# Performance work log

Measured on AMD Instinct MI355X. Metric: run time of the kernel, lower is better.

## Reference

```python
import jax, jax.numpy as jnp
import numpy as np

B, T, C = 4, 2048, 1024
H = 16
D = C // H  # head_dim = 64

def setup_inputs() -> dict:
    key = jax.random.key(0)
    k1, k2, k3 = jax.random.split(key, 3)
    x = jax.random.normal(k1, (B, T, C), dtype=jnp.float32)
    Wqkv = jax.random.normal(k2, (C, 3 * C), dtype=jnp.float32) * (C ** -0.5)
    Wproj = jax.random.normal(k3, (C, C), dtype=jnp.float32) * (C ** -0.5)
    return {"x": x, "Wqkv": Wqkv, "Wproj": Wproj}

def reference(x, Wqkv, Wproj):
    b, t, c = x.shape
    qkv = (x @ Wqkv).reshape(b, t, 3, H, D)
    qkv = jnp.transpose(qkv, (2, 0, 3, 1, 4))  # [3, B, H, T, D]
    q, k, v = qkv[0], qkv[1], qkv[2]
    att = jnp.einsum('bhqd,bhkd->bhqk', q, k) * (D ** -0.5)
    causal = jnp.tril(jnp.ones((t, t), dtype=bool))  # True where allowed
    att = jnp.where(causal, att, -jnp.inf)
    att = jax.nn.softmax(att, axis=-1)
    out = jnp.einsum('bhqk,bhkd->bhqd', att, v)  # [B, H, T, D]
    out = jnp.transpose(out, (0, 2, 1, 3)).reshape(b, t, c)
    return out @ Wproj
```

## Files before the change

kernel.cpp:

```cpp
#include <hip/hip_runtime.h>
#include <stdint.h>

typedef unsigned short u16;
typedef __bf16 bf16x8 __attribute__((ext_vector_type(8)));
typedef float f32x4 __attribute__((ext_vector_type(4)));

#define DEVI static __device__ __forceinline__

DEVI u16 f2bf(float f) {
  union { float f; unsigned u; } v; v.f = f;
  unsigned r = v.u + 0x7FFF + ((v.u >> 16) & 1);
  return (u16)(r >> 16);
}

DEVI unsigned pkbf(float a, float b) {
  union { float f; unsigned u; } x, y; x.f = a; y.f = b;
  return __builtin_amdgcn_perm(y.u + 0x8000u, x.u + 0x8000u, 0x07060302u);
}

DEVI unsigned cvtpk(float lo, float hi) {
  unsigned r;
  asm("v_cvt_pk_bf16_f32 %0, %1, %2" : "=v"(r) : "v"(lo), "v"(hi));
  return r;
}

DEVI void lds_fence() { asm volatile("s_waitcnt lgkmcnt(0)" ::: "memory"); }

DEVI void gl2lds16(const u16* g, u16* l) {
  __builtin_amdgcn_global_load_lds(
      (const __attribute__((address_space(1))) unsigned int*)(uintptr_t)g,
      (__attribute__((address_space(3))) unsigned int*)(uintptr_t)l,
      16, 0, 0);
}

__global__ __launch_bounds__(256)
void prep(const float* __restrict__ x, u16* __restrict__ xb,
          const float* __restrict__ Wqkv, u16* __restrict__ wqkvT,
          const float* __restrict__ Wproj, u16* __restrict__ wprojT) {
  __shared__ float tile[64][65];
  const int blk = blockIdx.x;
  if (blk < 8192) {
    const int i = blk * 256 + threadIdx.x;
    const float4 v = ((const float4*)x)[i];
    ushort4 o;
    o.x = f2bf(v.x); o.y = f2bf(v.y); o.z = f2bf(v.z); o.w = f2bf(v.w);
    ((ushort4*)xb)[i] = o;
    return;
  }
  const float* in; u16* out; int Cn, n0, r0;
  if (blk < 8960) {
    const int p = blk - 8192;
    in = Wqkv; out = wqkvT; Cn = 3072;
    n0 = (p % 48) * 64; r0 = (p / 48) * 64;
  } else {
    const int p = blk - 8960;
    in = Wproj; out = wprojT; Cn = 1024;
    n0 = (p % 16) * 64; r0 = (p / 16) * 64;
  }
#pragma unroll
  for (int i = 0; i < 16; ++i) {
    const int e = threadIdx.x + i * 256;
    const int r = e >> 6, c = e & 63;
    tile[r][c] = in[(size_t)(r0 + r) * Cn + n0 + c];
  }
  __syncthreads();
#pragma unroll
  for (int i = 0; i < 16; ++i) {
    const int e = threadIdx.x + i * 256;
    const int r = e >> 6, c = e & 63;
    out[(size_t)(n0 + r) * 1024 + r0 + c] = f2bf(tile[c][r]);
  }
}

template <int MODE>
__global__ __launch_bounds__(256)
void gemm128(const u16* __restrict__ A, const u16* __restrict__ Bt,
             int M, int N, int K, float* __restrict__ Cout,
             u16* __restrict__ Qg, u16* __restrict__ Kg, u16* __restrict__ Vtg) {
  __shared__ alignas(16) u16 As0[128 * 32];
  __shared__ alignas(16) u16 As1[128 * 32];
  __shared__ alignas(16) u16 Bs0[128 * 32];
  __shared__ alignas(16) u16 Bs1[128 * 32];
  const int tid = threadIdx.x;
  const int wave = tid >> 6, lane = tid & 63;
  const int quad = lane >> 4, l15 = lane & 15;
  const int m0 = blockIdx.y * 128;
  const int n0 = blockIdx.x * 128;
  const int wm = (wave >> 1) * 64;
  const int wn = (wave & 1) * 64;

  f32x4 acc[4][4] = {};

  const int q1 = wave * 64 + lane;
  const int q2 = q1 + 256;
  const int r1 = q1 >> 2, c1 = q1 & 3;
  const int r2 = q2 >> 2, c2 = q2 & 3;
  const size_t ga1 = (size_t)(m0 + r1) * K + c1 * 8;
  const size_t ga2 = (size_t)(m0 + r2) * K + c2 * 8;
  const size_t gb1 = (size_t)(n0 + r1) * K + c1 * 8;
  const size_t gb2 = (size_t)(n0 + r2) * K + c2 * 8;

  for (int k0 = 0; k0 < K; k0 += 64) {
    __syncthreads();
    gl2lds16(A + ga1 + k0, As0 + wave * 512);
    gl2lds16(A + ga2 + k0, As0 + 2048 + wave * 512);
    gl2lds16(Bt + gb1 + k0, Bs0 + wave * 512);
    gl2lds16(Bt + gb2 + k0, Bs0 + 2048 + wave * 512);
    gl2lds16(A + ga1 + k0 + 32, As1 + wave * 512);
    gl2lds16(A + ga2 + k0 + 32, As1 + 2048 + wave * 512);
    gl2lds16(Bt + gb1 + k0 + 32, Bs1 + wave * 512);
    gl2lds16(Bt + gb2 + k0 + 32, Bs1 + 2048 + wave * 512);
    __syncthreads();
#pragma unroll
    for (int kh = 0; kh < 2; ++kh) {
      const u16* Asl = kh ? As1 : As0;
      const u16* Bsl = kh ? Bs1 : Bs0;
      bf16x8 av[4], bv[4];
#pragma unroll
      for (int i = 0; i < 4; ++i)
        av[i] = *(const bf16x8*)(Asl + (wm + i * 16 + l15) * 32 + quad * 8);
#pragma unroll
      for (int j = 0; j < 4; ++j)
        bv[j] = *(const bf16x8*)(Bsl + (wn + j * 16 + l15) * 32 + quad * 8);
#pragma unroll
      for (int i = 0; i < 4; ++i)
#pragma unroll
        for (int j = 0; j < 4; ++j)
          acc[i][j] = __builtin_amdgcn_mfma_f32_16x16x32_bf16(av[i], bv[j], acc[i][j], 0, 0, 0);
    }
  }

  if constexpr (MODE == 0) {
#pragma unroll
    for (int i = 0; i < 4; ++i) {
#pragma unroll
      for (int j = 0; j < 4; ++j) {
        const int mb = m0 + wm + i * 16 + quad * 4;
        const int n = n0 + wn + j * 16 + l15;
#pragma unroll
        for (int r = 0; r < 4; ++r)
          Cout[(size_t)(mb + r) * N + n] = acc[i][j][r];
      }
    }
  } else {
    const int s0b = n0 >> 10;
    const int b = m0 >> 11;
    const int h = ((n0 + wn) >> 6) & 15;
    const int bh = b * 16 + h;
    const int tbase = (m0 & 2047) + wm;
    if (s0b == 2) {
      __syncthreads();
      u16* sl = (wave < 2 ? As0 : Bs0) + (wave & 1) * 2048;
#pragma unroll
      for (int jp = 0; jp < 2; ++jp) {
#pragma unroll
        for (int j2 = 0; j2 < 2; ++j2) {
          const int j = jp * 2 + j2;
          const int dl = j2 * 16 + l15;
          const int sw8 = dl & 7;
#pragma unroll
          for (int i = 0; i < 4; ++i) {
            const int tq = i * 2 + (quad >> 1);
            ushort4 pk;
            pk.x = f2bf(acc[i][j][0]); pk.y = f2bf(acc[i][j][1]);
            pk.z = f2bf(acc[i][j][2]); pk.w = f2bf(acc[i][j][3]);
            *(ushort4*)(sl + dl * 64 + ((tq ^ sw8) << 3) + (quad & 1) * 4) = pk;
          }
        }
        lds_fence();
#pragma unroll
        for (int p = 0; p < 4; ++p) {
          const int dl = p * 8 + (lane >> 3);
          const int tc = lane & 7;
          const int tcu = tc ^ (dl & 7);
          const uint4 v = *(const uint4*)(sl + dl * 64 + tc * 8);
          *(uint4*)(Vtg + ((size_t)(bh * 64 + jp * 32 + dl)) * 2048 + tbase + tcu * 8) = v;
        }
        lds_fence();
      }
    } else {
      u16* dst = s0b ? Kg : Qg;
      const float scale = s0b ? 1.0f : 0.18033688f;
#pragma unroll
      for (int i = 0; i < 4; ++i) {
        const int t0 = tbase + i * 16 + quad * 4;
#pragma unroll
        for (int j = 0; j < 4; ++j) {
          const int d = j * 16 + l15;
#pragma unroll
          for (int r = 0; r < 4; ++r)
            dst[((size_t)bh * 2048 + t0 + r) * 64 + d] = f2bf(acc[i][j][r] * scale);
        }
      }
    }
  }
}

__global__ __launch_bounds__(256)
void attn_fwd(const u16* __restrict__ Qg, const u16* __restrict__ Kg,
              const u16* __restrict__ Vtg, u16* __restrict__ Og) {
  __shared__ alignas(16) u16 Ks[2][64 * 64];
  __shared__ alignas(16) u16 Vts[2][64 * 64];
  __shared__ alignas(16) u16 Ps[4][16 * 64];

  const int tid = threadIdx.x;
  const int wave = tid >> 6, lane = tid & 63;
  const int quad = lane >> 4, l15 = lane & 15;
  const int bh = blockIdx.x & 63;
  const int qt = 15 - (blockIdx.x >> 6);
  const int b = bh >> 4, h = bh & 15;
  const int sw = l15 & 7;

  const int rs0 = wave * 16 + (lane >> 3);
  const int rs1 = rs0 + 8;
  const int cs = (lane & 7) ^ (rs0 & 7);
  const size_t kgb0 = (size_t)(bh * 2048 + rs0) * 64 + cs * 8;
  const size_t kgb1 = (size_t)(bh * 2048 + rs1) * 64 + cs * 8;
  const size_t vgb0 = (size_t)(bh * 64 + rs0) * 2048 + cs * 8;
  const size_t vgb1 = (size_t)(bh * 64 + rs1) * 2048 + cs * 8;
  const int ldsw0 = wave * 1024;
  const int ldsw1 = wave * 1024 + 512;

  const int qb0 = qt * 128 + wave * 32;

  bf16x8 bq[2][2];
#pragma unroll
  for (int qs = 0; qs < 2; ++qs)
#pragma unroll
    for (int hv = 0; hv < 2; ++hv)
      bq[qs][hv] = *(const bf16x8*)(Qg + ((size_t)bh * 2048 + qb0 + qs * 16 + l15) * 64 + hv * 32 + quad * 8);

  const __bf16 onebf = (__bf16)1.0f;
  const bf16x8 bONE = {onebf, onebf, onebf, onebf, onebf, onebf, onebf, onebf};

  f32x4 oacc[2][4] = {};
  f32x4 lacc[2] = {};

  const int jlast = qt * 128 + 64;
  const int nt = (jlast >> 6) + 1;

  gl2lds16(Kg + kgb0, Ks[0] + ldsw0);
  gl2lds16(Kg + kgb1, Ks[0] + ldsw1);
  gl2lds16(Vtg + vgb0, Vts[0] + ldsw0);
  gl2lds16(Vtg + vgb1, Vts[0] + ldsw1);
  asm volatile("s_waitcnt vmcnt(0)" ::: "memory");
  __builtin_amdgcn_s_barrier();

  for (int t = 0; t < nt; ++t) {
    const int j0 = t << 6;
    const int cur = t & 1;
    if (t + 1 < nt) {
      const size_t ko = (size_t)(j0 + 64) * 64;
      gl2lds16(Kg + kgb0 + ko, Ks[cur ^ 1] + ldsw0);
      gl2lds16(Kg + kgb1 + ko, Ks[cur ^ 1] + ldsw1);
      gl2lds16(Vtg + vgb0 + j0 + 64, Vts[cur ^ 1] + ldsw0);
      gl2lds16(Vtg + vgb1 + j0 + 64, Vts[cur ^ 1] + ldsw1);
    }

    if (j0 <= qb0 + 31) {
      __builtin_amdgcn_s_setprio(1);
      const u16* Kc = Ks[cur];
      const u16* Vc = Vts[cur];
      bf16x8 aK[4][2];
#pragma unroll
      for (int ks = 0; ks < 4; ++ks)
#pragma unroll
        for (int hv = 0; hv < 2; ++hv)
          aK[ks][hv] = *(const bf16x8*)(Kc + (ks * 16 + l15) * 64 + ((hv * 4 + quad) ^ sw) * 8);
      bf16x8 bV[4][2];
#pragma unroll
      for (int ds = 0; ds < 4; ++ds)
#pragma unroll
        for (int kc = 0; kc < 2; ++kc)
          bV[ds][kc] = *(const bf16x8*)(Vc + (ds * 16 + l15) * 64 + ((kc * 4 + quad) ^ sw) * 8);

#pragma unroll
      for (int qs = 0; qs < 2; ++qs) {
        const int qb = qb0 + qs * 16;
        if (j0 > qb + 15) continue;
        u16* Pw = Ps[wave];
        const bool needmask = (j0 + 63 > qb);
#pragma unroll
        for (int ks = 0; ks < 4; ++ks) {
          f32x4 s = {};
          s = __builtin_amdgcn_mfma_f32_16x16x32_bf16(aK[ks][0], bq[qs][0], s, 0, 0, 0);
          s = __builtin_amdgcn_mfma_f32_16x16x32_bf16(aK[ks][1], bq[qs][1], s, 0, 0, 0);
          if (needmask) {
            const int kbase = j0 + ks * 16 + quad * 4;
            const int qrow = qb + l15;
#pragma unroll
            for (int r = 0; r < 4; ++r)
              if (kbase + r > qrow) s[r] = -1e30f;
          }
          const float p0 = __builtin_amdgcn_exp2f(s[0]);
          const float p1 = __builtin_amdgcn_exp2f(s[1]);
          const float p2 = __builtin_amdgcn_exp2f(s[2]);
          const float p3 = __builtin_amdgcn_exp2f(s[3]);
          uint2 pk;
          pk.x = cvtpk(p0, p1);
          pk.y = cvtpk(p2, p3);
          *(uint2*)(Pw + l15 * 64 + (((ks * 2 + (quad >> 1)) ^ sw) * 8) + (quad & 1) * 4) = pk;
        }
        lds_fence();
        bf16x8 aP0 = *(const bf16x8*)(Pw + l15 * 64 + ((0 * 4 + quad) ^ sw) * 8);
        bf16x8 aP1 = *(const bf16x8*)(Pw + l15 * 64 + ((1 * 4 + quad) ^ sw) * 8);
        lacc[qs] = __builtin_amdgcn_mfma_f32_16x16x32_bf16(aP0, bONE, lacc[qs], 0, 0, 0);
        lacc[qs] = __builtin_amdgcn_mfma_f32_16x16x32_bf16(aP1, bONE, lacc[qs], 0, 0, 0);
#pragma unroll
        for (int ds = 0; ds < 4; ++ds) {
          oacc[qs][ds] = __builtin_amdgcn_mfma_f32_16x16x32_bf16(aP0, bV[ds][0], oacc[qs][ds], 0, 0, 0);
          oacc[qs][ds] = __builtin_amdgcn_mfma_f32_16x16x32_bf16(aP1, bV[ds][1], oacc[qs][ds], 0, 0, 0);
        }
      }
      __builtin_amdgcn_s_setprio(0);
    }

    asm volatile("s_waitcnt vmcnt(0)" ::: "memory");
    __builtin_amdgcn_s_barrier();
  }

#pragma unroll
  for (int qs = 0; qs < 2; ++qs) {
    const int qb = qb0 + qs * 16;
#pragma unroll
    for (int r = 0; r < 4; ++r) {
      const float inv = 1.0f / lacc[qs][r];
      u16* orow = Og + ((size_t)b * 2048 + qb + quad * 4 + r) * 1024 + h * 64;
#pragma unroll
      for (int ds = 0; ds < 4; ++ds)
        orow[ds * 16 + l15] = f2bf(oacc[qs][ds][r] * inv);
    }
  }
}

extern "C" void kernel_launch(void* const* d_in, const int* in_sizes, int n_in,
                              void* d_out, int out_size, void* d_ws, size_t ws_size,
                              hipStream_t stream) {
  const float* x = (const float*)d_in[0];
  const float* Wqkv = (const float*)d_in[1];
  const float* Wproj = (const float*)d_in[2];
  float* out = (float*)d_out;

  char* ws = (char*)d_ws;
  u16* xb     = (u16*)(ws);
  u16* wqkvT  = (u16*)(ws + 16777216);
  u16* wprojT = (u16*)(ws + 23068672);
  u16* Qg     = (u16*)(ws + 25165824);
  u16* Kg     = (u16*)(ws + 41943040);
  u16* Vtg    = (u16*)(ws + 58720256);
  u16* Og     = (u16*)(ws + 75497472);

  prep<<<9216, 256, 0, stream>>>(x, xb, Wqkv, wqkvT, Wproj, wprojT);
  gemm128<1><<<dim3(24, 64), 256, 0, stream>>>(xb, wqkvT, 8192, 3072, 1024,
                                               nullptr, Qg, Kg, Vtg);
  attn_fwd<<<1024, 256, 0, stream>>>(Qg, Kg, Vtg, Og);
  gemm128<0><<<dim3(8, 64), 256, 0, stream>>>(Og, wprojT, 8192, 1024, 1024,
                                              out, nullptr, nullptr, nullptr);
}
```

Measured before the change: 240.2 us.

## Load K/V directly from global into registers per wave, drop shared K/V staging

```diff
diff --git a/kernel.cpp b/kernel.cpp
--- a/kernel.cpp
+++ b/kernel.cpp
@@ -199,9 +199,7 @@
 __global__ __launch_bounds__(256)
 void attn_fwd(const u16* __restrict__ Qg, const u16* __restrict__ Kg,
               const u16* __restrict__ Vtg, u16* __restrict__ Og) {
-  __shared__ alignas(16) u16 Ks[2][64 * 64];
-  __shared__ alignas(16) u16 Vts[2][64 * 64];
-  __shared__ alignas(16) u16 Ps[4][16 * 64];
+  __shared__ alignas(16) u16 Ps[4][2][16 * 64];
 
   const int tid = threadIdx.x;
   const int wave = tid >> 6, lane = tid & 63;
@@ -211,17 +209,11 @@
   const int b = bh >> 4, h = bh & 15;
   const int sw = l15 & 7;
 
-  const int rs0 = wave * 16 + (lane >> 3);
-  const int rs1 = rs0 + 8;
-  const int cs = (lane & 7) ^ (rs0 & 7);
-  const size_t kgb0 = (size_t)(bh * 2048 + rs0) * 64 + cs * 8;
-  const size_t kgb1 = (size_t)(bh * 2048 + rs1) * 64 + cs * 8;
-  const size_t vgb0 = (size_t)(bh * 64 + rs0) * 2048 + cs * 8;
-  const size_t vgb1 = (size_t)(bh * 64 + rs1) * 2048 + cs * 8;
-  const int ldsw0 = wave * 1024;
-  const int ldsw1 = wave * 1024 + 512;
-
   const int qb0 = qt * 128 + wave * 32;
+  const int ntw = (qb0 >> 6) + 1;
+
+  const u16* Kb = Kg + (size_t)bh * 2048 * 64;
+  const u16* Vb = Vtg + (size_t)bh * 64 * 2048;
 
   bf16x8 bq[2][2];
 #pragma unroll
@@ -236,87 +228,115 @@
   f32x4 oacc[2][4] = {};
   f32x4 lacc[2] = {};
 
-  const int jlast = qt * 128 + 64;
-  const int nt = (jlast >> 6) + 1;
-
-  gl2lds16(Kg + kgb0, Ks[0] + ldsw0);
-  gl2lds16(Kg + kgb1, Ks[0] + ldsw1);
-  gl2lds16(Vtg + vgb0, Vts[0] + ldsw0);
-  gl2lds16(Vtg + vgb1, Vts[0] + ldsw1);
-  asm volatile("s_waitcnt vmcnt(0)" ::: "memory");
-  __builtin_amdgcn_s_barrier();
-
-  for (int t = 0; t < nt; ++t) {
+  bf16x8 aK[4][2];
+#pragma unroll
+  for (int ks = 0; ks < 4; ++ks)
+#pragma unroll
+    for (int hv = 0; hv < 2; ++hv)
+      aK[ks][hv] = *(const bf16x8*)(Kb + (size_t)(ks * 16 + l15) * 64 + hv * 32 + quad * 8);
+
+  u16* Pw0 = Ps[wave][0];
+  u16* Pw1 = Ps[wave][1];
+
+  for (int t = 0; t < ntw; ++t) {
     const int j0 = t << 6;
-    const int cur = t & 1;
-    if (t + 1 < nt) {
-      const size_t ko = (size_t)(j0 + 64) * 64;
-      gl2lds16(Kg + kgb0 + ko, Ks[cur ^ 1] + ldsw0);
-      gl2lds16(Kg + kgb1 + ko, Ks[cur ^ 1] + ldsw1);
-      gl2lds16(Vtg + vgb0 + j0 + 64, Vts[cur ^ 1] + ldsw0);
-      gl2lds16(Vtg + vgb1 + j0 + 64, Vts[cur ^ 1] + ldsw1);
-    }
-
-    if (j0 <= qb0 + 31) {
-      __builtin_amdgcn_s_setprio(1);
-      const u16* Kc = Ks[cur];
-      const u16* Vc = Vts[cur];
-      bf16x8 aK[4][2];
-#pragma unroll
-      for (int ks = 0; ks < 4; ++ks)
-#pragma unroll
-        for (int hv = 0; hv < 2; ++hv)
-          aK[ks][hv] = *(const bf16x8*)(Kc + (ks * 16 + l15) * 64 + ((hv * 4 + quad) ^ sw) * 8);
-      bf16x8 bV[4][2];
-#pragma unroll
-      for (int ds = 0; ds < 4; ++ds)
-#pragma unroll
-        for (int kc = 0; kc < 2; ++kc)
-          bV[ds][kc] = *(const bf16x8*)(Vc + (ds * 16 + l15) * 64 + ((kc * 4 + quad) ^ sw) * 8);
-
-#pragma unroll
-      for (int qs = 0; qs < 2; ++qs) {
-        const int qb = qb0 + qs * 16;
-        if (j0 > qb + 15) continue;
-        u16* Pw = Ps[wave];
-        const bool needmask = (j0 + 63 > qb);
-#pragma unroll
-        for (int ks = 0; ks < 4; ++ks) {
-          f32x4 s = {};
-          s = __builtin_amdgcn_mfma_f32_16x16x32_bf16(aK[ks][0], bq[qs][0], s, 0, 0, 0);
-          s = __builtin_amdgcn_mfma_f32_16x16x32_bf16(aK[ks][1], bq[qs][1], s, 0, 0, 0);
-          if (needmask) {
-            const int kbase = j0 + ks * 16 + quad * 4;
-            const int qrow = qb + l15;
-#pragma unroll
-            for (int r = 0; r < 4; ++r)
-              if (kbase + r > qrow) s[r] = -1e30f;
-          }
-          const float p0 = __builtin_amdgcn_exp2f(s[0]);
-          const float p1 = __builtin_amdgcn_exp2f(s[1]);
-          const float p2 = __builtin_amdgcn_exp2f(s[2]);
-          const float p3 = __builtin_amdgcn_exp2f(s[3]);
-          uint2 pk;
-          pk.x = cvtpk(p0, p1);
-          pk.y = cvtpk(p2, p3);
-          *(uint2*)(Pw + l15 * 64 + (((ks * 2 + (quad >> 1)) ^ sw) * 8) + (quad & 1) * 4) = pk;
-        }
-        lds_fence();
-        bf16x8 aP0 = *(const bf16x8*)(Pw + l15 * 64 + ((0 * 4 + quad) ^ sw) * 8);
-        bf16x8 aP1 = *(const bf16x8*)(Pw + l15 * 64 + ((1 * 4 + quad) ^ sw) * 8);
-        lacc[qs] = __builtin_amdgcn_mfma_f32_16x16x32_bf16(aP0, bONE, lacc[qs], 0, 0, 0);
-        lacc[qs] = __builtin_amdgcn_mfma_f32_16x16x32_bf16(aP1, bONE, lacc[qs], 0, 0, 0);
-#pragma unroll
-        for (int ds = 0; ds < 4; ++ds) {
-          oacc[qs][ds] = __builtin_amdgcn_mfma_f32_16x16x32_bf16(aP0, bV[ds][0], oacc[qs][ds], 0, 0, 0);
-          oacc[qs][ds] = __builtin_amdgcn_mfma_f32_16x16x32_bf16(aP1, bV[ds][1], oacc[qs][ds], 0, 0, 0);
-        }
-      }
-      __builtin_amdgcn_s_setprio(0);
-    }
-
-    asm volatile("s_waitcnt vmcnt(0)" ::: "memory");
-    __builtin_amdgcn_s_barrier();
+    bf16x8 bV[4][2];
+#pragma unroll
+    for (int ds = 0; ds < 4; ++ds)
+#pragma unroll
+      for (int kc = 0; kc < 2; ++kc)
+        bV[ds][kc] = *(const bf16x8*)(Vb + (size_t)(ds * 16 + l15) * 2048 + j0 + kc * 32 + quad * 8);
+
+    {
+      const int qb = qb0;
+      const bool needmask = (j0 + 63 > qb);
+#pragma unroll
+      for (int ks = 0; ks < 4; ++ks) {
+        f32x4 s = {};
+        s = __builtin_amdgcn_mfma_f32_16x16x32_bf16(aK[ks][0], bq[0][0], s, 0, 0, 0);
+        s = __builtin_amdgcn_mfma_f32_16x16x32_bf16(aK[ks][1], bq[0][1], s, 0, 0, 0);
+        if (needmask) {
+          const int kbase = j0 + ks * 16 + quad * 4;
+          const int qrow = qb + l15;
+#pragma unroll
+          for (int r = 0; r < 4; ++r)
+            if (kbase + r > qrow) s[r] = -1e30f;
+        }
+        const float p0 = __builtin_amdgcn_exp2f(s[0]);
+        const float p1 = __builtin_amdgcn_exp2f(s[1]);
+        const float p2 = __builtin_amdgcn_exp2f(s[2]);
+        const float p3 = __builtin_amdgcn_exp2f(s[3]);
+        uint2 pk;
+        pk.x = cvtpk(p0, p1);
+        pk.y = cvtpk(p2, p3);
+        *(uint2*)(Pw0 + l15 * 64 + (((ks * 2 + (quad >> 1)) ^ sw) * 8) + (quad & 1) * 4) = pk;
+      }
+    }
+
+    {
+      const int qb = qb0 + 16;
+      const bool needmask = (j0 + 63 > qb);
+      f32x4 s4[4];
+#pragma unroll
+      for (int ks = 0; ks < 4; ++ks) {
+        f32x4 s = {};
+        s = __builtin_amdgcn_mfma_f32_16x16x32_bf16(aK[ks][0], bq[1][0], s, 0, 0, 0);
+        s = __builtin_amdgcn_mfma_f32_16x16x32_bf16(aK[ks][1], bq[1][1], s, 0, 0, 0);
+        s4[ks] = s;
+      }
+      if (t + 1 < ntw) {
+        const int j1 = j0 + 64;
+#pragma unroll
+        for (int ks = 0; ks < 4; ++ks)
+#pragma unroll
+          for (int hv = 0; hv < 2; ++hv)
+            aK[ks][hv] = *(const bf16x8*)(Kb + (size_t)(j1 + ks * 16 + l15) * 64 + hv * 32 + quad * 8);
+      }
+#pragma unroll
+      for (int ks = 0; ks < 4; ++ks) {
+        f32x4 s = s4[ks];
+        if (needmask) {
+          const int kbase = j0 + ks * 16 + quad * 4;
+          const int qrow = qb + l15;
+#pragma unroll
+          for (int r = 0; r < 4; ++r)
+            if (kbase + r > qrow) s[r] = -1e30f;
+        }
+        const float p0 = __builtin_amdgcn_exp2f(s[0]);
+        const float p1 = __builtin_amdgcn_exp2f(s[1]);
+        const float p2 = __builtin_amdgcn_exp2f(s[2]);
+        const float p3 = __builtin_amdgcn_exp2f(s[3]);
+        uint2 pk;
+        pk.x = cvtpk(p0, p1);
+        pk.y = cvtpk(p2, p3);
+        *(uint2*)(Pw1 + l15 * 64 + (((ks * 2 + (quad >> 1)) ^ sw) * 8) + (quad & 1) * 4) = pk;
+      }
+    }
+
+    lds_fence();
+
+    {
+      bf16x8 aP0 = *(const bf16x8*)(Pw0 + l15 * 64 + ((0 * 4 + quad) ^ sw) * 8);
+      bf16x8 aP1 = *(const bf16x8*)(Pw0 + l15 * 64 + ((1 * 4 + quad) ^ sw) * 8);
+      lacc[0] = __builtin_amdgcn_mfma_f32_16x16x32_bf16(aP0, bONE, lacc[0], 0, 0, 0);
+      lacc[0] = __builtin_amdgcn_mfma_f32_16x16x32_bf16(aP1, bONE, lacc[0], 0, 0, 0);
+#pragma unroll
+      for (int ds = 0; ds < 4; ++ds) {
+        oacc[0][ds] = __builtin_amdgcn_mfma_f32_16x16x32_bf16(aP0, bV[ds][0], oacc[0][ds], 0, 0, 0);
+        oacc[0][ds] = __builtin_amdgcn_mfma_f32_16x16x32_bf16(aP1, bV[ds][1], oacc[0][ds], 0, 0, 0);
+      }
+    }
+    {
+      bf16x8 aP0 = *(const bf16x8*)(Pw1 + l15 * 64 + ((0 * 4 + quad) ^ sw) * 8);
+      bf16x8 aP1 = *(const bf16x8*)(Pw1 + l15 * 64 + ((1 * 4 + quad) ^ sw) * 8);
+      lacc[1] = __builtin_amdgcn_mfma_f32_16x16x32_bf16(aP0, bONE, lacc[1], 0, 0, 0);
+      lacc[1] = __builtin_amdgcn_mfma_f32_16x16x32_bf16(aP1, bONE, lacc[1], 0, 0, 0);
+#pragma unroll
+      for (int ds = 0; ds < 4; ++ds) {
+        oacc[1][ds] = __builtin_amdgcn_mfma_f32_16x16x32_bf16(aP0, bV[ds][0], oacc[1][ds], 0, 0, 0);
+        oacc[1][ds] = __builtin_amdgcn_mfma_f32_16x16x32_bf16(aP1, bV[ds][1], oacc[1][ds], 0, 0, 0);
+      }
+    }
   }
 
 #pragma unroll
```

Result: slower. 314.4 us (+30.9%).

## Enlarge GEMM block tile to 256x128 with 8 waves sharing B tile

Applied to the files above, without the earlier changes.

```diff
diff --git a/kernel.cpp b/kernel.cpp
--- a/kernel.cpp
+++ b/kernel.cpp
@@ -11,11 +11,6 @@
   union { float f; unsigned u; } v; v.f = f;
   unsigned r = v.u + 0x7FFF + ((v.u >> 16) & 1);
   return (u16)(r >> 16);
-}
-
-DEVI unsigned pkbf(float a, float b) {
-  union { float f; unsigned u; } x, y; x.f = a; y.f = b;
-  return __builtin_amdgcn_perm(y.u + 0x8000u, x.u + 0x8000u, 0x07060302u);
 }
 
 DEVI unsigned cvtpk(float lo, float hi) {
@@ -73,43 +68,41 @@
 }
 
 template <int MODE>
-__global__ __launch_bounds__(256)
+__global__ __launch_bounds__(512)
 void gemm128(const u16* __restrict__ A, const u16* __restrict__ Bt,
              int M, int N, int K, float* __restrict__ Cout,
              u16* __restrict__ Qg, u16* __restrict__ Kg, u16* __restrict__ Vtg) {
-  __shared__ alignas(16) u16 As0[128 * 32];
-  __shared__ alignas(16) u16 As1[128 * 32];
+  __shared__ alignas(16) u16 As0[256 * 32];
+  __shared__ alignas(16) u16 As1[256 * 32];
   __shared__ alignas(16) u16 Bs0[128 * 32];
   __shared__ alignas(16) u16 Bs1[128 * 32];
   const int tid = threadIdx.x;
   const int wave = tid >> 6, lane = tid & 63;
   const int quad = lane >> 4, l15 = lane & 15;
-  const int m0 = blockIdx.y * 128;
+  const int m0 = blockIdx.y * 256;
   const int n0 = blockIdx.x * 128;
   const int wm = (wave >> 1) * 64;
   const int wn = (wave & 1) * 64;
 
   f32x4 acc[4][4] = {};
 
-  const int q1 = wave * 64 + lane;
-  const int q2 = q1 + 256;
-  const int r1 = q1 >> 2, c1 = q1 & 3;
-  const int r2 = q2 >> 2, c2 = q2 & 3;
-  const size_t ga1 = (size_t)(m0 + r1) * K + c1 * 8;
-  const size_t ga2 = (size_t)(m0 + r2) * K + c2 * 8;
-  const size_t gb1 = (size_t)(n0 + r1) * K + c1 * 8;
-  const size_t gb2 = (size_t)(n0 + r2) * K + c2 * 8;
+  const int qA0 = wave * 64 + lane;
+  const int qA1 = qA0 + 512;
+  const int rA0 = qA0 >> 2, cA0 = qA0 & 3;
+  const int rA1 = qA1 >> 2, cA1 = qA1 & 3;
+  const int rB = qA0 >> 2, cB = qA0 & 3;
+  const size_t gaA0 = (size_t)(m0 + rA0) * K + cA0 * 8;
+  const size_t gaA1 = (size_t)(m0 + rA1) * K + cA1 * 8;
+  const size_t gbB  = (size_t)(n0 + rB) * K + cB * 8;
 
   for (int k0 = 0; k0 < K; k0 += 64) {
     __syncthreads();
-    gl2lds16(A + ga1 + k0, As0 + wave * 512);
-    gl2lds16(A + ga2 + k0, As0 + 2048 + wave * 512);
-    gl2lds16(Bt + gb1 + k0, Bs0 + wave * 512);
-    gl2lds16(Bt + gb2 + k0, Bs0 + 2048 + wave * 512);
-    gl2lds16(A + ga1 + k0 + 32, As1 + wave * 512);
-    gl2lds16(A + ga2 + k0 + 32, As1 + 2048 + wave * 512);
-    gl2lds16(Bt + gb1 + k0 + 32, Bs1 + wave * 512);
-    gl2lds16(Bt + gb2 + k0 + 32, Bs1 + 2048 + wave * 512);
+    gl2lds16(A + gaA0 + k0, As0 + wave * 512);
+    gl2lds16(A + gaA1 + k0, As0 + 4096 + wave * 512);
+    gl2lds16(Bt + gbB + k0, Bs0 + wave * 512);
+    gl2lds16(A + gaA0 + k0 + 32, As1 + wave * 512);
+    gl2lds16(A + gaA1 + k0 + 32, As1 + 4096 + wave * 512);
+    gl2lds16(Bt + gbB + k0 + 32, Bs1 + wave * 512);
     __syncthreads();
 #pragma unroll
     for (int kh = 0; kh < 2; ++kh) {
@@ -150,7 +143,7 @@
     const int tbase = (m0 & 2047) + wm;
     if (s0b == 2) {
       __syncthreads();
-      u16* sl = (wave < 2 ? As0 : Bs0) + (wave & 1) * 2048;
+      u16* sl = (wave < 4 ? As0 : As1) + (wave & 3) * 2048;
 #pragma unroll
       for (int jp = 0; jp < 2; ++jp) {
 #pragma unroll
@@ -351,9 +344,9 @@
   u16* Og     = (u16*)(ws + 75497472);
 
   prep<<<9216, 256, 0, stream>>>(x, xb, Wqkv, wqkvT, Wproj, wprojT);
-  gemm128<1><<<dim3(24, 64), 256, 0, stream>>>(xb, wqkvT, 8192, 3072, 1024,
+  gemm128<1><<<dim3(24, 32), 512, 0, stream>>>(xb, wqkvT, 8192, 3072, 1024,
                                                nullptr, Qg, Kg, Vtg);
   attn_fwd<<<1024, 256, 0, stream>>>(Qg, Kg, Vtg, Og);
-  gemm128<0><<<dim3(8, 64), 256, 0, stream>>>(Og, wprojT, 8192, 1024, 1024,
+  gemm128<0><<<dim3(8, 32), 512, 0, stream>>>(Og, wprojT, 8192, 1024, 1024,
                                               out, nullptr, nullptr, nullptr);
 }
```

New measurement: 254.2 us. 1.06x slower.
